# Performance work log

Hardware: AMD Instinct MI355X
Metric: run time of the kernel (lower is better)

Reference implementation:

```python
import jax, jax.numpy as jnp
import numpy as np

N_NODES = 50000
N_EDGES = 800000
D_IN = 128
D_OUT = 64


def setup_inputs() -> dict:
    key = jax.random.key(0)
    k1, k2, k3, k4 = jax.random.split(key, 4)
    x = jax.random.normal(k1, (N_NODES, D_IN), dtype=jnp.float32)
    W = jax.random.normal(k2, (D_OUT, D_IN), dtype=jnp.float32) * (1.0 / np.sqrt(D_IN))
    b = jnp.zeros((D_OUT,), dtype=jnp.float32)
    row = jax.random.randint(k3, (N_EDGES,), 0, N_NODES, dtype=jnp.int32)
    col = jax.random.randint(k4, (N_EDGES,), 0, N_NODES, dtype=jnp.int32)
    return {"x": x, "W": W, "b": b, "row": row, "col": col}


def reference(x, W, b, row, col):
    # Linear projection: [N, D_in] -> [N, D_out]
    h = x @ W.T + b
    n = x.shape[0]
    # Row-normalized SpMM: out[i] = (1/deg(i)) * sum_{(i,j) in E} h[j]
    msg = h[col]  # gather source features: [E, D_out]
    summed = jax.ops.segment_sum(msg, row, num_segments=n)
    deg = jax.ops.segment_sum(jnp.ones_like(row, dtype=h.dtype), row, num_segments=n)
    out = summed / jnp.maximum(deg, 1.0)[:, None]
    return out
```

## Files before the change

### kernel.cpp

```cpp
#include <hip/hip_runtime.h>
#include <hip/hip_bf16.h>

#define D_IN   128
#define D_OUT  64
#define CAP    64
#define MAX_USHORT_NODES 65536
#define BIN_SHIFT 6
#define MAX_BINS  1024
#define BIN_CAP   4096
#define P1_BLOCKS 256
#define FAT_THREADS 512

using frag_ab = __attribute__((ext_vector_type(8))) short;
using frag_cd = __attribute__((ext_vector_type(4))) float;
using vfloat4 = __attribute__((ext_vector_type(4))) float;

static __device__ __forceinline__ short f2bf(float f) {
    union { float f; unsigned u; } v; v.f = f;
    unsigned r = v.u + 0x7FFFu + ((v.u >> 16) & 1u);
    return (short)(r >> 16);
}
static __device__ __forceinline__ float bflo(unsigned w) {
    union { unsigned u; float f; } v; v.u = w << 16; return v.f;
}
static __device__ __forceinline__ float bfhi(unsigned w) {
    union { unsigned u; float f; } v; v.u = w & 0xFFFF0000u; return v.f;
}

__global__ __launch_bounds__(FAT_THREADS)
void proj_bin1_kernel(const float* __restrict__ x,
                      const float* __restrict__ W,
                      const float* __restrict__ bvec,
                      unsigned short* __restrict__ h,
                      const int* __restrict__ row, const int* __restrict__ col,
                      unsigned* __restrict__ scratch, int* __restrict__ cursor,
                      int* __restrict__ ovfA_cnt, unsigned* __restrict__ ovfA_list,
                      int ovfA_cap, int n_nodes, int n_edges, int n_bins) {
    __shared__ int hist[MAX_BINS];
    __shared__ int base[MAX_BINS];

    if ((int)blockIdx.x < P1_BLOCKS) {
        const int per = (n_edges + P1_BLOCKS - 1) / P1_BLOCKS;
        const int e0 = (int)blockIdx.x * per;
        const int e1 = min(e0 + per, n_edges);

        for (int i = threadIdx.x; i < n_bins; i += FAT_THREADS) hist[i] = 0;
        __syncthreads();
        for (int e = e0 + (int)threadIdx.x; e < e1; e += FAT_THREADS)
            atomicAdd(&hist[row[e] >> BIN_SHIFT], 1);
        __syncthreads();
        for (int i = threadIdx.x; i < n_bins; i += FAT_THREADS) {
            const int hcnt = hist[i];
            base[i] = hcnt > 0 ? atomicAdd(&cursor[i * 16], hcnt) : 0;
            hist[i] = 0;
        }
        __syncthreads();
        for (int e = e0 + (int)threadIdx.x; e < e1; e += FAT_THREADS) {
            const int r = row[e];
            const int c = col[e];
            const int bn = r >> BIN_SHIFT;
            const int loc = atomicAdd(&hist[bn], 1);
            const int off = base[bn] + loc;
            if (off < BIN_CAP) {
                scratch[(size_t)bn * BIN_CAP + off] =
                    (unsigned)(r & 63) | ((unsigned)c << 6);
            } else {
                const int k = atomicAdd(ovfA_cnt, 1);
                if (k < ovfA_cap) ovfA_list[k] = (unsigned)r | ((unsigned)c << 16);
            }
        }
        return;
    }

    const int lane = (int)threadIdx.x & 63;
    const int wid  = (int)(((blockIdx.x - P1_BLOCKS) * blockDim.x + threadIdx.x) >> 6);
    const int nwaves = (int)(((gridDim.x - P1_BLOCKS) * blockDim.x) >> 6);
    const int m    = lane & 15;
    const int quad = lane >> 4;

    frag_ab Bf[4][4];
#pragma unroll
    for (int kk = 0; kk < 4; ++kk) {
#pragma unroll
        for (int nt = 0; nt < 4; ++nt) {
            const float* wp = W + (size_t)(nt * 16 + m) * D_IN + kk * 32 + quad * 8;
            const float4 w0 = *(const float4*)wp;
            const float4 w1 = *(const float4*)(wp + 4);
            frag_ab f;
            f[0] = f2bf(w0.x); f[1] = f2bf(w0.y); f[2] = f2bf(w0.z); f[3] = f2bf(w0.w);
            f[4] = f2bf(w1.x); f[5] = f2bf(w1.y); f[6] = f2bf(w1.z); f[7] = f2bf(w1.w);
            Bf[kk][nt] = f;
        }
    }
    float bb[4];
#pragma unroll
    for (int nt = 0; nt < 4; ++nt) bb[nt] = bvec[nt * 16 + m];

    const int ntiles = (n_nodes + 15) / 16;
    for (int tile = wid; tile < ntiles; tile += nwaves) {
        const int node_base = tile * 16;
        int arow = node_base + m;
        if (arow > n_nodes - 1) arow = n_nodes - 1;

        vfloat4 xv[8];
        const float* xr = x + (size_t)arow * D_IN + quad * 8;
#pragma unroll
        for (int kk = 0; kk < 4; ++kk) {
            xv[2 * kk]     = __builtin_nontemporal_load((const vfloat4*)(xr + kk * 32));
            xv[2 * kk + 1] = __builtin_nontemporal_load((const vfloat4*)(xr + kk * 32 + 4));
        }

        frag_cd acc[4];
#pragma unroll
        for (int nt = 0; nt < 4; ++nt) {
            acc[nt][0] = bb[nt]; acc[nt][1] = bb[nt];
            acc[nt][2] = bb[nt]; acc[nt][3] = bb[nt];
        }
#pragma unroll
        for (int kk = 0; kk < 4; ++kk) {
            const vfloat4 x0 = xv[2 * kk], x1 = xv[2 * kk + 1];
            frag_ab A;
            A[0] = f2bf(x0.x); A[1] = f2bf(x0.y); A[2] = f2bf(x0.z); A[3] = f2bf(x0.w);
            A[4] = f2bf(x1.x); A[5] = f2bf(x1.y); A[6] = f2bf(x1.z); A[7] = f2bf(x1.w);
#pragma unroll
            for (int nt = 0; nt < 4; ++nt)
                acc[nt] = __builtin_amdgcn_mfma_f32_16x16x32_bf16(A, Bf[kk][nt],
                                                                  acc[nt], 0, 0, 0);
        }
#pragma unroll
        for (int nt = 0; nt < 4; ++nt) {
#pragma unroll
            for (int r = 0; r < 4; ++r) {
                const int node = node_base + quad * 4 + r;
                if (node < n_nodes)
                    h[(size_t)node * D_OUT + nt * 16 + m] =
                        (unsigned short)f2bf(acc[nt][r]);
            }
        }
    }
}

__global__ __launch_bounds__(FAT_THREADS)
void bin_gather_kernel(const unsigned* __restrict__ scratch,
                       const int* __restrict__ cursor,
                       const uint2* __restrict__ h64,
                       int* __restrict__ deg,
                       const unsigned* __restrict__ ovfA_list,
                       const int* __restrict__ ovfA_cnt, int ovfA_cap,
                       int* __restrict__ ovfB_cnt, unsigned* __restrict__ ovfB_list,
                       int ovfB_cap,
                       float* __restrict__ out, int n_nodes) {
    __shared__ int ldeg[64];
    __shared__ unsigned short lbuck[64 * CAP];
    const int bin   = (int)blockIdx.x;
    const int node0 = bin << BIN_SHIFT;

    int cnt = cursor[bin * 16]; if (cnt > BIN_CAP) cnt = BIN_CAP;

    if (threadIdx.x < 64) ldeg[threadIdx.x] = 0;
    __syncthreads();

    for (int i = threadIdx.x; i < cnt; i += FAT_THREADS) {
        const unsigned rec = scratch[(size_t)bin * BIN_CAP + i];
        const int rl = (int)(rec & 63u);
        const int s = atomicAdd(&ldeg[rl], 1);
        if (s < CAP) {
            lbuck[(rl << 6) + s] = (unsigned short)(rec >> 6);
        } else {
            const int k = atomicAdd(ovfB_cnt, 1);
            if (k < ovfB_cap)
                ovfB_list[k] = (unsigned)(node0 + rl) | ((rec >> 6) << 16);
        }
    }
    int cA = *ovfA_cnt; if (cA > ovfA_cap) cA = ovfA_cap;
    for (int i = threadIdx.x; i < cA; i += FAT_THREADS) {
        const unsigned rec = ovfA_list[i];
        const int r = (int)(rec & 0xFFFFu);
        if ((r >> BIN_SHIFT) == bin) atomicAdd(&ldeg[r & 63], 1);
    }
    __syncthreads();

    if (threadIdx.x < 64 && node0 + (int)threadIdx.x < n_nodes)
        deg[node0 + threadIdx.x] = ldeg[threadIdx.x];

    const int lane = (int)threadIdx.x & 63;
    const int q = lane >> 4;
    const int j = lane & 15;
    const int w = (int)threadIdx.x >> 6;

    for (int r6 = w; r6 < 64; r6 += 8) {
        const int node = node0 + r6;
        if (node >= n_nodes) continue;
        const int d = ldeg[r6];
        const int dc = d < CAP ? d : CAP;
        const int ngr = (dc + 3) >> 2;
        const unsigned short* brow = &lbuck[r6 << 6];

        float a0 = 0.f, a1 = 0.f, a2 = 0.f, a3 = 0.f;
        float b0 = 0.f, b1 = 0.f, b2 = 0.f, b3 = 0.f;
        int g = 0;
        for (; g + 2 <= ngr; g += 2) {
            const int iA = (int)brow[4 * g + q];
            const int iB = (int)brow[4 * g + 4 + q];
            uint2 wA = h64[(size_t)iA * 16 + j];
            uint2 wB = h64[(size_t)iB * 16 + j];
            if (4 * g + q >= dc)     { wA.x = 0u; wA.y = 0u; }
            if (4 * g + 4 + q >= dc) { wB.x = 0u; wB.y = 0u; }
            a0 += bflo(wA.x); a1 += bfhi(wA.x); a2 += bflo(wA.y); a3 += bfhi(wA.y);
            b0 += bflo(wB.x); b1 += bfhi(wB.x); b2 += bflo(wB.y); b3 += bfhi(wB.y);
        }
        for (; g < ngr; ++g) {
            const int iA = (int)brow[4 * g + q];
            uint2 wA = h64[(size_t)iA * 16 + j];
            if (4 * g + q >= dc) { wA.x = 0u; wA.y = 0u; }
            a0 += bflo(wA.x); a1 += bfhi(wA.x); a2 += bflo(wA.y); a3 += bfhi(wA.y);
        }
        a0 += b0; a1 += b1; a2 += b2; a3 += b3;
        a0 += __shfl_xor(a0, 16); a0 += __shfl_xor(a0, 32);
        a1 += __shfl_xor(a1, 16); a1 += __shfl_xor(a1, 32);
        a2 += __shfl_xor(a2, 16); a2 += __shfl_xor(a2, 32);
        a3 += __shfl_xor(a3, 16); a3 += __shfl_xor(a3, 32);
        if (q == 0) {
            const float inv = 1.0f / fmaxf((float)d, 1.0f);
            vfloat4 o;
            o.x = a0 * inv; o.y = a1 * inv; o.z = a2 * inv; o.w = a3 * inv;
            __builtin_nontemporal_store(
                o, (vfloat4*)(out + (size_t)node * D_OUT + j * 4));
        }
    }
}

__global__ void ovf_apply_kernel(const unsigned short* __restrict__ h,
                                 const int* __restrict__ deg,
                                 const unsigned* __restrict__ listA,
                                 const int* __restrict__ cntA_p, int capA,
                                 const unsigned* __restrict__ listB,
                                 const int* __restrict__ cntB_p, int capB,
                                 float* __restrict__ out) {
    int cA = *cntA_p; if (cA > capA) cA = capA;
    int cB = *cntB_p; if (cB > capB) cB = capB;
    const long long n_tasks = (long long)(cA + cB) * D_OUT;
    long long t = (long long)blockIdx.x * blockDim.x + threadIdx.x;
    const long long stride = (long long)gridDim.x * blockDim.x;
    for (; t < n_tasks; t += stride) {
        const int k = (int)(t >> 6);
        const int lane = (int)(t & 63);
        const unsigned rec = (k < cA) ? listA[k] : listB[k - cA];
        const int r = (int)(rec & 0xFFFFu);
        const int c = (int)(rec >> 16);
        union { unsigned u; float f; } v;
        v.u = ((unsigned)h[(size_t)c * D_OUT + lane]) << 16;
        atomicAdd(&out[(size_t)r * D_OUT + lane],
                  v.f / fmaxf((float)deg[r], 1.0f));
    }
}

__global__ void proj_only_kernel(const float* __restrict__ x,
                                 const float* __restrict__ W,
                                 const float* __restrict__ bvec,
                                 float* __restrict__ h, int n_nodes) {
    const int lane = (int)threadIdx.x & 63;
    const int wave = (int)((blockIdx.x * blockDim.x + threadIdx.x) >> 6);
    const int nwaves = (int)((gridDim.x * blockDim.x) >> 6);
    const float bias = bvec[lane];
    for (int node = wave; node < n_nodes; node += nwaves) {
        const float* xr = &x[(size_t)node * D_IN];
        float acc = bias;
#pragma unroll
        for (int k = 0; k < D_IN; ++k) acc += xr[k] * W[lane * D_IN + k];
        h[(size_t)node * D_OUT + lane] = acc;
    }
}

__global__ void scatter_kernel(const float* __restrict__ h,
                               const int* __restrict__ row,
                               const int* __restrict__ col,
                               float* __restrict__ out,
                               int* __restrict__ deg,
                               long long n_tasks) {
    long long t = (long long)blockIdx.x * blockDim.x + threadIdx.x;
    const long long stride = (long long)gridDim.x * blockDim.x;
    for (; t < n_tasks; t += stride) {
        const int e = (int)(t >> 6);
        const int c = (int)(t & 63);
        atomicAdd(&out[(size_t)row[e] * D_OUT + c], h[(size_t)col[e] * D_OUT + c]);
        if (c == 0) atomicAdd(&deg[row[e]], 1);
    }
}

__global__ void div_kernel(float* __restrict__ out,
                           const int* __restrict__ deg, int n_total) {
    int t = blockIdx.x * blockDim.x + threadIdx.x;
    if (t < n_total) {
        out[t] *= 1.0f / fmaxf((float)deg[t >> 6], 1.0f);
    }
}

extern "C" void kernel_launch(void* const* d_in, const int* in_sizes, int n_in,
                              void* d_out, int out_size, void* d_ws, size_t ws_size,
                              hipStream_t stream) {
    const float* x   = (const float*)d_in[0];
    const float* W   = (const float*)d_in[1];
    const float* b   = (const float*)d_in[2];
    const int*   row = (const int*)d_in[3];
    const int*   col = (const int*)d_in[4];
    float* out = (float*)d_out;

    const int n_nodes = in_sizes[0] / D_IN;
    const int n_edges = in_sizes[3];
    const int n_bins  = (n_nodes + 63) >> BIN_SHIFT;

    char* p = (char*)d_ws;
    unsigned short* h = (unsigned short*)p;
    p += (size_t)n_nodes * D_OUT * sizeof(unsigned short);
    int* deg = (int*)p;            p += (size_t)n_nodes * sizeof(int);
    int* ovf_cnts = (int*)p;       p += 256;
    int* cursor = (int*)p;         p += (size_t)MAX_BINS * 16 * sizeof(int);
    unsigned* ovfA_list = (unsigned*)p;  p += (size_t)n_edges * sizeof(unsigned);
    unsigned* ovfB_list = (unsigned*)p;  p += (size_t)n_edges * sizeof(unsigned);
    unsigned* scratch = (unsigned*)p;
    p += (size_t)n_bins * BIN_CAP * sizeof(unsigned);
    const size_t needed = (size_t)(p - (char*)d_ws);

    if (ws_size >= needed && n_nodes <= MAX_USHORT_NODES) {
        hipMemsetAsync(ovf_cnts, 0, 256 + (size_t)n_bins * 16 * sizeof(int),
                       stream);

        const int ntiles = (n_nodes + 15) / 16;
        int proj_blocks = (ntiles + 15) / 16;
        if (proj_blocks < 1) proj_blocks = 1;
        proj_bin1_kernel<<<P1_BLOCKS + proj_blocks, FAT_THREADS, 0, stream>>>(
            x, W, b, h, row, col, scratch, cursor, &ovf_cnts[0], ovfA_list,
            n_edges, n_nodes, n_edges, n_bins);

        bin_gather_kernel<<<n_bins, FAT_THREADS, 0, stream>>>(
            scratch, cursor, (const uint2*)h, deg, ovfA_list, &ovf_cnts[0],
            n_edges, &ovf_cnts[1], ovfB_list, n_edges, out, n_nodes);

        ovf_apply_kernel<<<256, 256, 0, stream>>>(h, deg, ovfA_list,
                                                  &ovf_cnts[0], n_edges,
                                                  ovfB_list, &ovf_cnts[1],
                                                  n_edges, out);
    } else {
        float* hf = (float*)d_ws;
        int* degf = (int*)((char*)d_ws + (size_t)n_nodes * D_OUT * sizeof(float));
        hipMemsetAsync(out, 0, (size_t)out_size * sizeof(float), stream);
        hipMemsetAsync(degf, 0, (size_t)n_nodes * sizeof(int), stream);
        proj_only_kernel<<<1024, 256, 0, stream>>>(x, W, b, hf, n_nodes);
        const long long n_tasks = (long long)n_edges * D_OUT;
        scatter_kernel<<<16384, 256, 0, stream>>>(hf, row, col, out, degf, n_tasks);
        const int n_total = n_nodes * D_OUT;
        div_kernel<<<(n_total + 255) / 256, 256, 0, stream>>>(out, degf, n_total);
    }
}
```

Before: 134.5 us.

## Fuse binning, projection, gather and overflow into one cooperative kernel

Replaces the memset plus three kernel launches with a single cooperative kernel of 256 blocks that uses grid-wide syncs between phases: zeroing counters, then binning and projection, then per-bin gather, then overflow apply. Binning now runs on 64 blocks with the remaining 192 doing the projection, and bins are walked in a grid-stride loop. This is meant to remove launch and inter-kernel gaps. In exchange it adds grid.sync barriers, lower parallelism per phase (256 blocks instead of 782 gather blocks), and drops the nontemporal loads and stores. The old multi-kernel path is kept as a fallback if the cooperative launch fails.

```diff
diff --git a/kernel.cpp b/kernel.cpp
--- a/kernel.cpp
+++ b/kernel.cpp
@@ -1,5 +1,8 @@
 #include <hip/hip_runtime.h>
 #include <hip/hip_bf16.h>
+#include <hip/hip_cooperative_groups.h>
+
+namespace cg = cooperative_groups;
 
 #define D_IN   128
 #define D_OUT  64
@@ -8,12 +11,12 @@
 #define BIN_SHIFT 6
 #define MAX_BINS  1024
 #define BIN_CAP   4096
-#define P1_BLOCKS 256
+#define FUSED_BLOCKS 256
+#define P1B 64
 #define FAT_THREADS 512
 
 using frag_ab = __attribute__((ext_vector_type(8))) short;
 using frag_cd = __attribute__((ext_vector_type(4))) float;
-using vfloat4 = __attribute__((ext_vector_type(4))) float;
 
 static __device__ __forceinline__ short f2bf(float f) {
     union { float f; unsigned u; } v; v.f = f;
@@ -27,11 +30,235 @@
     union { unsigned u; float f; } v; v.u = w & 0xFFFF0000u; return v.f;
 }
 
+static __device__ __forceinline__ void proj_body(
+        const float* __restrict__ x, const float* __restrict__ W,
+        const float* __restrict__ bvec, unsigned short* __restrict__ h,
+        int n_nodes, int wid, int nwaves, int lane) {
+    const int m    = lane & 15;
+    const int quad = lane >> 4;
+
+    frag_ab Bf[4][4];
+#pragma unroll
+    for (int kk = 0; kk < 4; ++kk) {
+#pragma unroll
+        for (int nt = 0; nt < 4; ++nt) {
+            const float* wp = W + (size_t)(nt * 16 + m) * D_IN + kk * 32 + quad * 8;
+            const float4 w0 = *(const float4*)wp;
+            const float4 w1 = *(const float4*)(wp + 4);
+            frag_ab f;
+            f[0] = f2bf(w0.x); f[1] = f2bf(w0.y); f[2] = f2bf(w0.z); f[3] = f2bf(w0.w);
+            f[4] = f2bf(w1.x); f[5] = f2bf(w1.y); f[6] = f2bf(w1.z); f[7] = f2bf(w1.w);
+            Bf[kk][nt] = f;
+        }
+    }
+    float bb[4];
+#pragma unroll
+    for (int nt = 0; nt < 4; ++nt) bb[nt] = bvec[nt * 16 + m];
+
+    const int ntiles = (n_nodes + 15) / 16;
+    for (int tile = wid; tile < ntiles; tile += nwaves) {
+        const int node_base = tile * 16;
+        int arow = node_base + m;
+        if (arow > n_nodes - 1) arow = n_nodes - 1;
+
+        float4 xv[8];
+        const float* xr = x + (size_t)arow * D_IN + quad * 8;
+#pragma unroll
+        for (int kk = 0; kk < 4; ++kk) {
+            xv[2 * kk]     = *(const float4*)(xr + kk * 32);
+            xv[2 * kk + 1] = *(const float4*)(xr + kk * 32 + 4);
+        }
+
+        frag_cd acc[4];
+#pragma unroll
+        for (int nt = 0; nt < 4; ++nt) {
+            acc[nt][0] = bb[nt]; acc[nt][1] = bb[nt];
+            acc[nt][2] = bb[nt]; acc[nt][3] = bb[nt];
+        }
+#pragma unroll
+        for (int kk = 0; kk < 4; ++kk) {
+            const float4 x0 = xv[2 * kk], x1 = xv[2 * kk + 1];
+            frag_ab A;
+            A[0] = f2bf(x0.x); A[1] = f2bf(x0.y); A[2] = f2bf(x0.z); A[3] = f2bf(x0.w);
+            A[4] = f2bf(x1.x); A[5] = f2bf(x1.y); A[6] = f2bf(x1.z); A[7] = f2bf(x1.w);
+#pragma unroll
+            for (int nt = 0; nt < 4; ++nt)
+                acc[nt] = __builtin_amdgcn_mfma_f32_16x16x32_bf16(A, Bf[kk][nt],
+                                                                  acc[nt], 0, 0, 0);
+        }
+#pragma unroll
+        for (int nt = 0; nt < 4; ++nt) {
+#pragma unroll
+            for (int r = 0; r < 4; ++r) {
+                const int node = node_base + quad * 4 + r;
+                if (node < n_nodes)
+                    h[(size_t)node * D_OUT + nt * 16 + m] =
+                        (unsigned short)f2bf(acc[nt][r]);
+            }
+        }
+    }
+}
+
 __global__ __launch_bounds__(FAT_THREADS)
-void proj_bin1_kernel(const float* __restrict__ x,
-                      const float* __restrict__ W,
-                      const float* __restrict__ bvec,
-                      unsigned short* __restrict__ h,
+void fused_kernel(const float* __restrict__ x, const float* __restrict__ W,
+                  const float* __restrict__ bvec, unsigned short* __restrict__ h,
+                  const int* __restrict__ row, const int* __restrict__ col,
+                  unsigned* __restrict__ scratch, int* __restrict__ cursor,
+                  int* __restrict__ ovf_cnts, unsigned* __restrict__ ovfA_list,
+                  unsigned* __restrict__ ovfB_list, int ovf_cap,
+                  int* __restrict__ deg, float* __restrict__ out,
+                  int n_nodes, int n_edges, int n_bins) {
+    __shared__ int hist[MAX_BINS];
+    __shared__ int base[MAX_BINS];
+    __shared__ int ldeg[64];
+    __shared__ unsigned short lbuck[64 * CAP];
+
+    cg::grid_group grid = cg::this_grid();
+    const int tid  = (int)threadIdx.x;
+    const int gtid = (int)(blockIdx.x * blockDim.x + threadIdx.x);
+    const int gsz  = (int)(gridDim.x * blockDim.x);
+    const uint2* h64 = (const uint2*)h;
+
+    for (int i = gtid; i < n_bins * 16; i += gsz) cursor[i] = 0;
+    if (gtid == 0) { ovf_cnts[0] = 0; ovf_cnts[1] = 0; }
+    grid.sync();
+
+    if ((int)blockIdx.x < P1B) {
+        const int per = (n_edges + P1B - 1) / P1B;
+        const int e0 = (int)blockIdx.x * per;
+        const int e1 = min(e0 + per, n_edges);
+
+        for (int i = tid; i < n_bins; i += FAT_THREADS) hist[i] = 0;
+        __syncthreads();
+        for (int e = e0 + tid; e < e1; e += FAT_THREADS)
+            atomicAdd(&hist[row[e] >> BIN_SHIFT], 1);
+        __syncthreads();
+        for (int i = tid; i < n_bins; i += FAT_THREADS) {
+            const int hcnt = hist[i];
+            base[i] = hcnt > 0 ? atomicAdd(&cursor[i * 16], hcnt) : 0;
+            hist[i] = 0;
+        }
+        __syncthreads();
+        for (int e = e0 + tid; e < e1; e += FAT_THREADS) {
+            const int r = row[e];
+            const int c = col[e];
+            const int bn = r >> BIN_SHIFT;
+            const int loc = atomicAdd(&hist[bn], 1);
+            const int off = base[bn] + loc;
+            if (off < BIN_CAP) {
+                scratch[(size_t)bn * BIN_CAP + off] =
+                    (unsigned)(r & 63) | ((unsigned)c << 6);
+            } else {
+                const int k = atomicAdd(&ovf_cnts[0], 1);
+                if (k < ovf_cap) ovfA_list[k] = (unsigned)r | ((unsigned)c << 16);
+            }
+        }
+    } else {
+        const int lane = tid & 63;
+        const int wid  = ((int)blockIdx.x - P1B) * (FAT_THREADS >> 6) + (tid >> 6);
+        const int nwaves = ((int)gridDim.x - P1B) * (FAT_THREADS >> 6);
+        proj_body(x, W, bvec, h, n_nodes, wid, nwaves, lane);
+    }
+    grid.sync();
+
+    const int lane = tid & 63;
+    const int q = lane >> 4;
+    const int j = lane & 15;
+    const int w = tid >> 6;
+    int cA = ovf_cnts[0]; if (cA > ovf_cap) cA = ovf_cap;
+
+    for (int bin = (int)blockIdx.x; bin < n_bins; bin += (int)gridDim.x) {
+        __syncthreads();
+        if (tid < 64) ldeg[tid] = 0;
+        __syncthreads();
+
+        const int node0 = bin << BIN_SHIFT;
+        int cnt = cursor[bin * 16]; if (cnt > BIN_CAP) cnt = BIN_CAP;
+
+        for (int i = tid; i < cnt; i += FAT_THREADS) {
+            const unsigned rec = scratch[(size_t)bin * BIN_CAP + i];
+            const int rl = (int)(rec & 63u);
+            const int s = atomicAdd(&ldeg[rl], 1);
+            if (s < CAP) {
+                lbuck[(rl << 6) + s] = (unsigned short)(rec >> 6);
+            } else {
+                const int k = atomicAdd(&ovf_cnts[1], 1);
+                if (k < ovf_cap)
+                    ovfB_list[k] = (unsigned)(node0 + rl) | ((rec >> 6) << 16);
+            }
+        }
+        for (int i = tid; i < cA; i += FAT_THREADS) {
+            const unsigned rec = ovfA_list[i];
+            const int r = (int)(rec & 0xFFFFu);
+            if ((r >> BIN_SHIFT) == bin) atomicAdd(&ldeg[r & 63], 1);
+        }
+        __syncthreads();
+
+        if (tid < 64 && node0 + tid < n_nodes) deg[node0 + tid] = ldeg[tid];
+
+        for (int r6 = w; r6 < 64; r6 += 8) {
+            const int node = node0 + r6;
+            if (node >= n_nodes) continue;
+            const int d = ldeg[r6];
+            const int dc = d < CAP ? d : CAP;
+            const int ngr = (dc + 3) >> 2;
+            const unsigned short* brow = &lbuck[r6 << 6];
+
+            float a0 = 0.f, a1 = 0.f, a2 = 0.f, a3 = 0.f;
+            float b0 = 0.f, b1 = 0.f, b2 = 0.f, b3 = 0.f;
+            int g = 0;
+            for (; g + 2 <= ngr; g += 2) {
+                const int iA = (int)brow[4 * g + q];
+                const int iB = (int)brow[4 * g + 4 + q];
+                uint2 wA = h64[(size_t)iA * 16 + j];
+                uint2 wB = h64[(size_t)iB * 16 + j];
+                if (4 * g + q >= dc)     { wA.x = 0u; wA.y = 0u; }
+                if (4 * g + 4 + q >= dc) { wB.x = 0u; wB.y = 0u; }
+                a0 += bflo(wA.x); a1 += bfhi(wA.x); a2 += bflo(wA.y); a3 += bfhi(wA.y);
+                b0 += bflo(wB.x); b1 += bfhi(wB.x); b2 += bflo(wB.y); b3 += bfhi(wB.y);
+            }
+            for (; g < ngr; ++g) {
+                const int iA = (int)brow[4 * g + q];
+                uint2 wA = h64[(size_t)iA * 16 + j];
+                if (4 * g + q >= dc) { wA.x = 0u; wA.y = 0u; }
+                a0 += bflo(wA.x); a1 += bfhi(wA.x); a2 += bflo(wA.y); a3 += bfhi(wA.y);
+            }
+            a0 += b0; a1 += b1; a2 += b2; a3 += b3;
+            a0 += __shfl_xor(a0, 16); a0 += __shfl_xor(a0, 32);
+            a1 += __shfl_xor(a1, 16); a1 += __shfl_xor(a1, 32);
+            a2 += __shfl_xor(a2, 16); a2 += __shfl_xor(a2, 32);
+            a3 += __shfl_xor(a3, 16); a3 += __shfl_xor(a3, 32);
+            if (q == 0) {
+                const float inv = 1.0f / fmaxf((float)d, 1.0f);
+                float4 o;
+                o.x = a0 * inv; o.y = a1 * inv; o.z = a2 * inv; o.w = a3 * inv;
+                *(float4*)(out + (size_t)node * D_OUT + j * 4) = o;
+            }
+        }
+    }
+    grid.sync();
+
+    cA = ovf_cnts[0]; if (cA > ovf_cap) cA = ovf_cap;
+    int cB = ovf_cnts[1]; if (cB > ovf_cap) cB = ovf_cap;
+    const long long n_tasks = (long long)(cA + cB) * D_OUT;
+    for (long long t = gtid; t < n_tasks; t += gsz) {
+        const int k = (int)(t >> 6);
+        const int ln = (int)(t & 63);
+        const unsigned rec = (k < cA) ? ovfA_list[k] : ovfB_list[k - cA];
+        const int r = (int)(rec & 0xFFFFu);
+        const int c = (int)(rec >> 16);
+        union { unsigned u; float f; } v;
+        v.u = ((unsigned)h[(size_t)c * D_OUT + ln]) << 16;
+        atomicAdd(&out[(size_t)r * D_OUT + ln],
+                  v.f / fmaxf((float)deg[r], 1.0f));
+    }
+}
+
+#define P1_BLOCKS 256
+
+__global__ __launch_bounds__(FAT_THREADS)
+void proj_bin1_kernel(const float* __restrict__ x, const float* __restrict__ W,
+                      const float* __restrict__ bvec, unsigned short* __restrict__ h,
                       const int* __restrict__ row, const int* __restrict__ col,
                       unsigned* __restrict__ scratch, int* __restrict__ cursor,
                       int* __restrict__ ovfA_cnt, unsigned* __restrict__ ovfA_list,
@@ -71,73 +298,11 @@
         }
         return;
     }
-
     const int lane = (int)threadIdx.x & 63;
-    const int wid  = (int)(((blockIdx.x - P1_BLOCKS) * blockDim.x + threadIdx.x) >> 6);
-    const int nwaves = (int)(((gridDim.x - P1_BLOCKS) * blockDim.x) >> 6);
-    const int m    = lane & 15;
-    const int quad = lane >> 4;
-
-    frag_ab Bf[4][4];
-#pragma unroll
-    for (int kk = 0; kk < 4; ++kk) {
-#pragma unroll
-        for (int nt = 0; nt < 4; ++nt) {
-            const float* wp = W + (size_t)(nt * 16 + m) * D_IN + kk * 32 + quad * 8;
-            const float4 w0 = *(const float4*)wp;
-            const float4 w1 = *(const float4*)(wp + 4);
-            frag_ab f;
-            f[0] = f2bf(w0.x); f[1] = f2bf(w0.y); f[2] = f2bf(w0.z); f[3] = f2bf(w0.w);
-            f[4] = f2bf(w1.x); f[5] = f2bf(w1.y); f[6] = f2bf(w1.z); f[7] = f2bf(w1.w);
-            Bf[kk][nt] = f;
-        }
-    }
-    float bb[4];
-#pragma unroll
-    for (int nt = 0; nt < 4; ++nt) bb[nt] = bvec[nt * 16 + m];
-
-    const int ntiles = (n_nodes + 15) / 16;
-    for (int tile = wid; tile < ntiles; tile += nwaves) {
-        const int node_base = tile * 16;
-        int arow = node_base + m;
-        if (arow > n_nodes - 1) arow = n_nodes - 1;
-
-        vfloat4 xv[8];
-        const float* xr = x + (size_t)arow * D_IN + quad * 8;
-#pragma unroll
-        for (int kk = 0; kk < 4; ++kk) {
-            xv[2 * kk]     = __builtin_nontemporal_load((const vfloat4*)(xr + kk * 32));
-            xv[2 * kk + 1] = __builtin_nontemporal_load((const vfloat4*)(xr + kk * 32 + 4));
-        }
-
-        frag_cd acc[4];
-#pragma unroll
-        for (int nt = 0; nt < 4; ++nt) {
-            acc[nt][0] = bb[nt]; acc[nt][1] = bb[nt];
-            acc[nt][2] = bb[nt]; acc[nt][3] = bb[nt];
-        }
-#pragma unroll
-        for (int kk = 0; kk < 4; ++kk) {
-            const vfloat4 x0 = xv[2 * kk], x1 = xv[2 * kk + 1];
-            frag_ab A;
-            A[0] = f2bf(x0.x); A[1] = f2bf(x0.y); A[2] = f2bf(x0.z); A[3] = f2bf(x0.w);
-            A[4] = f2bf(x1.x); A[5] = f2bf(x1.y); A[6] = f2bf(x1.z); A[7] = f2bf(x1.w);
-#pragma unroll
-            for (int nt = 0; nt < 4; ++nt)
-                acc[nt] = __builtin_amdgcn_mfma_f32_16x16x32_bf16(A, Bf[kk][nt],
-                                                                  acc[nt], 0, 0, 0);
-        }
-#pragma unroll
-        for (int nt = 0; nt < 4; ++nt) {
-#pragma unroll
-            for (int r = 0; r < 4; ++r) {
-                const int node = node_base + quad * 4 + r;
-                if (node < n_nodes)
-                    h[(size_t)node * D_OUT + nt * 16 + m] =
-                        (unsigned short)f2bf(acc[nt][r]);
-            }
-        }
-    }
+    const int wid  = ((int)blockIdx.x - P1_BLOCKS) * (FAT_THREADS >> 6)
+                   + ((int)threadIdx.x >> 6);
+    const int nwaves = ((int)gridDim.x - P1_BLOCKS) * (FAT_THREADS >> 6);
+    proj_body(x, W, bvec, h, n_nodes, wid, nwaves, lane);
 }
 
 __global__ __launch_bounds__(FAT_THREADS)
@@ -222,10 +387,9 @@
         a3 += __shfl_xor(a3, 16); a3 += __shfl_xor(a3, 32);
         if (q == 0) {
             const float inv = 1.0f / fmaxf((float)d, 1.0f);
-            vfloat4 o;
+            float4 o;
             o.x = a0 * inv; o.y = a1 * inv; o.z = a2 * inv; o.w = a3 * inv;
-            __builtin_nontemporal_store(
-                o, (vfloat4*)(out + (size_t)node * D_OUT + j * 4));
+            *(float4*)(out + (size_t)node * D_OUT + j * 4) = o;
         }
     }
 }
@@ -323,20 +487,30 @@
     const size_t needed = (size_t)(p - (char*)d_ws);
 
     if (ws_size >= needed && n_nodes <= MAX_USHORT_NODES) {
+        int ovf_cap = n_edges;
+        void* args[] = {
+            (void*)&x, (void*)&W, (void*)&b, (void*)&h, (void*)&row, (void*)&col,
+            (void*)&scratch, (void*)&cursor, (void*)&ovf_cnts, (void*)&ovfA_list,
+            (void*)&ovfB_list, (void*)&ovf_cap, (void*)&deg, (void*)&out,
+            (void*)&n_nodes, (void*)&n_edges, (void*)&n_bins
+        };
+        hipError_t err = hipLaunchCooperativeKernel(
+            (const void*)fused_kernel, dim3(FUSED_BLOCKS), dim3(FAT_THREADS),
+            args, 0, stream);
+        if (err == hipSuccess) return;
+        (void)hipGetLastError();
+
         hipMemsetAsync(ovf_cnts, 0, 256 + (size_t)n_bins * 16 * sizeof(int),
                        stream);
-
         const int ntiles = (n_nodes + 15) / 16;
         int proj_blocks = (ntiles + 15) / 16;
         if (proj_blocks < 1) proj_blocks = 1;
         proj_bin1_kernel<<<P1_BLOCKS + proj_blocks, FAT_THREADS, 0, stream>>>(
             x, W, b, h, row, col, scratch, cursor, &ovf_cnts[0], ovfA_list,
             n_edges, n_nodes, n_edges, n_bins);
-
         bin_gather_kernel<<<n_bins, FAT_THREADS, 0, stream>>>(
             scratch, cursor, (const uint2*)h, deg, ovfA_list, &ovf_cnts[0],
             n_edges, &ovf_cnts[1], ovfB_list, n_edges, out, n_nodes);
-
         ovf_apply_kernel<<<256, 256, 0, stream>>>(h, deg, ovfA_list,
                                                   &ovf_cnts[0], n_edges,
                                                   ovfB_list, &ovf_cnts[1],
```

After: 241.5 us. +79.5%, slower.
